# Kernel optimization log

Hardware: AMD Instinct MI355X
Metric: run time of the kernel (lower is better)

Reference implementation:

```python
import jax, jax.numpy as jnp
import numpy as np

H = 2048      # hidden_size
DM = 4096     # intermediate_size
N = 16        # ssm state size
K = 4         # conv kernel
R = 128       # time_step_rank
B_SZ = 1
L = 1024


def setup_inputs() -> dict:
    key = jax.random.key(0)
    ks = jax.random.split(key, 10)
    s = 0.02
    hidden_states = jax.random.normal(ks[0], (B_SZ, L, H), dtype=jnp.float32)
    W_in = jax.random.normal(ks[1], (2 * DM, H), dtype=jnp.float32) * s
    conv_w = jax.random.normal(ks[2], (DM, 1, K), dtype=jnp.float32) * 0.3
    conv_b = jax.random.normal(ks[3], (DM,), dtype=jnp.float32) * 0.1
    W_x = jax.random.normal(ks[4], (R + 2 * N, DM), dtype=jnp.float32) * s
    W_dt = jax.random.normal(ks[5], (DM, R), dtype=jnp.float32) * s
    b_dt = jax.random.normal(ks[6], (DM,), dtype=jnp.float32) * 0.1
    # A_log init: log(arange(1..N)) broadcast over channels (per __init__)
    A_log = jnp.broadcast_to(jnp.log(jnp.arange(1, N + 1, dtype=jnp.float32))[None, :], (DM, N)).copy()
    D_param = jnp.ones((DM,), dtype=jnp.float32)
    W_out = jax.random.normal(ks[7], (H, DM), dtype=jnp.float32) * s
    return {"hidden_states": hidden_states, "W_in": W_in, "conv_w": conv_w,
            "conv_b": conv_b, "W_x": W_x, "W_dt": W_dt, "b_dt": b_dt,
            "A_log": A_log, "D_param": D_param, "W_out": W_out}


def reference(hidden_states, W_in, conv_w, conv_b, W_x, W_dt, b_dt, A_log, D_param, W_out):
    # in_proj then chunk into hidden / gate (torch chunks dim=1 after transpose)
    proj = hidden_states @ W_in.T                     # [B, L, 2D]
    h, gate = proj[..., :DM], proj[..., DM:]          # each [B, L, D]
    # depthwise causal conv1d, padding K-1 then truncate to L (left-pad == same)
    h_cl = jnp.transpose(h, (0, 2, 1))                # [B, D, L]
    hc = jax.lax.conv_general_dilated(
        h_cl, conv_w, window_strides=(1,), padding=[(K - 1, 0)],
        dimension_numbers=("NCH", "OIH", "NCH"), feature_group_count=DM)
    hc = jax.nn.silu(hc + conv_b[None, :, None])      # [B, D, L]
    hc_ld = jnp.transpose(hc, (0, 2, 1))              # [B, L, D]
    # x_proj -> dt, B, C
    ssm_p = hc_ld @ W_x.T                             # [B, L, R+2N]
    ts, Bm, Cm = ssm_p[..., :R], ssm_p[..., R:R + N], ssm_p[..., R + N:]
    dt = jax.nn.softplus(ts @ W_dt.T + b_dt)          # [B, L, D]
    A = -jnp.exp(A_log)                               # [D, N]
    dA = jnp.exp(dt[:, :, :, None] * A[None, None, :, :])            # [B, L, D, N]
    dBu = dt[:, :, :, None] * Bm[:, :, None, :] * hc_ld[:, :, :, None]  # [B, L, D, N]
    # selective scan over time: state = dA*state + dBu; y = <state, C>
    def step(state, inp):
        dA_t, dBu_t, C_t = inp                        # [B,D,N],[B,D,N],[B,N]
        state = dA_t * state + dBu_t
        y = jnp.einsum("bdn,bn->bd", state, C_t)
        return state, y
    init = jnp.zeros((hidden_states.shape[0], DM, N), dtype=hidden_states.dtype)
    _, ys = jax.lax.scan(step, init,
                         (jnp.swapaxes(dA, 0, 1), jnp.swapaxes(dBu, 0, 1), jnp.swapaxes(Cm, 0, 1)))
    y = jnp.transpose(ys, (1, 0, 2))                  # [B, L, D]
    y = y + hc_ld * D_param[None, None, :]            # skip via D
    y = y * jax.nn.silu(gate)                         # gating
    return y @ W_out.T                                # [B, L, H]
```

## Files before the change

### kernel.cpp

```cpp
#include <hip/hip_runtime.h>
#include <math.h>

#define AS1 __attribute__((address_space(1)))
#define AS3 __attribute__((address_space(3)))

typedef __attribute__((ext_vector_type(8))) short short8;
typedef __attribute__((ext_vector_type(4))) float f32x4;

#define WAITV(n) asm volatile("s_waitcnt vmcnt(" #n ")" ::: "memory")
#define BARRIER() asm volatile("s_barrier" ::: "memory")

static __device__ __forceinline__ unsigned short f2bf(float f) {
    unsigned u = __float_as_uint(f);
    unsigned r = (u + 0x7fffu + ((u >> 16) & 1u)) >> 16;
    return (unsigned short)r;
}

__global__ __launch_bounds__(256) void cvt_f32_bf16(const float* __restrict__ src,
                                                    unsigned short* __restrict__ dst,
                                                    int n4) {
    int i = blockIdx.x * 256 + threadIdx.x;
    int stride = gridDim.x * 256;
    for (; i < n4; i += stride) {
        float4 v = ((const float4*)src)[i];
        ushort4 o;
        o.x = f2bf(v.x); o.y = f2bf(v.y); o.z = f2bf(v.z); o.w = f2bf(v.w);
        ((ushort4*)dst)[i] = o;
    }
}

__global__ __launch_bounds__(256) void cvt_ts(const float* __restrict__ ssmp,
                                              unsigned short* __restrict__ ts) {
    int i = blockIdx.x * 256 + threadIdx.x;
    int t = i >> 5, c4 = (i & 31) * 4;
    float4 v = *(const float4*)&ssmp[t * 160 + c4];
    ushort4 o;
    o.x = f2bf(v.x); o.y = f2bf(v.y); o.z = f2bf(v.z); o.w = f2bf(v.w);
    *(ushort4*)&ts[t * 128 + c4] = o;
}

__global__ __launch_bounds__(256) void conv_silu(const float* __restrict__ h,
                                                 const float* __restrict__ cw,
                                                 const float* __restrict__ cb,
                                                 float* __restrict__ hc_f,
                                                 unsigned short* __restrict__ hc_bf) {
    int idx = blockIdx.x * 256 + threadIdx.x;
    int d = idx & 4095, t = idx >> 12;
    float acc = cb[d];
    float4 w = *(const float4*)&cw[d * 4];
    const float* wp = (const float*)&w;
#pragma unroll
    for (int k = 0; k < 4; ++k) {
        int tt = t + k - 3;
        if (tt >= 0) acc += h[tt * 4096 + d] * wp[k];
    }
    float s = acc / (1.f + __expf(-acc));
    hc_f[idx] = s;
    hc_bf[idx] = f2bf(s);
}

enum { P_SPLIT = 0, P_ATOMIC = 1 };

template <int EPI>
__global__ __launch_bounds__(512, 2)
void gemm8p(const short* __restrict__ A, const short* __restrict__ B,
            float* __restrict__ C0, float* __restrict__ C1,
            int N, int K, int kchunk) {
    __shared__ short lds[2 * 24576];

    const int tid = threadIdx.x;
    const int wv = tid >> 6, ln = tid & 63;
    const int lr = ln & 15, kg = ln >> 4;
    const int wm = wv >> 2, wn = wv & 3;

    const int nwg = gridDim.x;
    const int bid = blockIdx.x;
    const int swz = (bid & 7) * (nwg >> 3) + (bid >> 3);
    const int by = swz & 7, bx = swz >> 3;
    const int m0 = by * 128;
    const int n0 = bx * 256;
    const int kbeg = blockIdx.z * kchunk;
    const int NT = kchunk >> 6;

    f32x4 acc[4][4];
#pragma unroll
    for (int mi = 0; mi < 4; ++mi)
#pragma unroll
        for (int ni = 0; ni < 4; ++ni) acc[mi][ni] = (f32x4){0.f, 0.f, 0.f, 0.f};

    const short* Abase = A + (size_t)m0 * K + kbeg;
    const short* Bbase = B + (size_t)n0 * K + kbeg;

#define STAGE(kt, b)                                                          \
    {                                                                         \
        short* lbase = &lds[(b) * 24576];                                     \
        _Pragma("unroll")                                                     \
        for (int r = 0; r < 2; ++r) {                                         \
            int c = r * 512 + tid;                                            \
            int row = c >> 3, cb8 = (c & 7) << 4;                             \
            int scb = cb8 ^ ((row & 7) << 4);                                 \
            const short* src = Abase + (size_t)row * K + (kt) * 64 + (scb >> 1); \
            short* dst = lbase + (r * 512 + wv * 64) * 8;                     \
            __builtin_amdgcn_global_load_lds((const AS1 void*)src,            \
                                             (AS3 void*)dst, 16, 0, 0);       \
        }                                                                     \
        _Pragma("unroll")                                                     \
        for (int r = 0; r < 4; ++r) {                                         \
            int c = r * 512 + tid;                                            \
            int row = c >> 3, cb8 = (c & 7) << 4;                             \
            int scb = cb8 ^ ((row & 7) << 4);                                 \
            const short* src = Bbase + (size_t)row * K + (kt) * 64 + (scb >> 1); \
            short* dst = lbase + 8192 + (r * 512 + wv * 64) * 8;              \
            __builtin_amdgcn_global_load_lds((const AS1 void*)src,            \
                                             (AS3 void*)dst, 16, 0, 0);       \
        }                                                                     \
    }

    STAGE(0, 0);

    for (int kt = 0; kt < NT; ++kt) {
        const int b = kt & 1;
        if (kt + 1 < NT) STAGE(kt + 1, b ^ 1);
        if (kt + 1 < NT) { WAITV(6); } else { WAITV(0); }
        BARRIER();
        {
            const short* la = &lds[b * 24576];
            const short* lb = la + 8192;
#pragma unroll
            for (int ks = 0; ks < 2; ++ks) {
                short8 av[4], bv[4];
#pragma unroll
                for (int mi = 0; mi < 4; ++mi) {
                    int row = wm * 64 + mi * 16 + lr;
                    int col = (ks * 32 + kg * 8) ^ ((row & 7) << 3);
                    av[mi] = *(const short8*)&la[row * 64 + col];
                }
#pragma unroll
                for (int ni = 0; ni < 4; ++ni) {
                    int row = wn * 64 + ni * 16 + lr;
                    int col = (ks * 32 + kg * 8) ^ ((row & 7) << 3);
                    bv[ni] = *(const short8*)&lb[row * 64 + col];
                }
                __builtin_amdgcn_s_setprio(1);
#pragma unroll
                for (int mi = 0; mi < 4; ++mi)
#pragma unroll
                    for (int ni = 0; ni < 4; ++ni)
                        acc[mi][ni] = __builtin_amdgcn_mfma_f32_16x16x32_bf16(
                            av[mi], bv[ni], acc[mi][ni], 0, 0, 0);
                __builtin_amdgcn_s_setprio(0);
            }
        }
        BARRIER();
    }
#undef STAGE

#pragma unroll
    for (int mi = 0; mi < 4; ++mi) {
        int crow0 = m0 + wm * 64 + mi * 16 + kg * 4;
#pragma unroll
        for (int ni = 0; ni < 4; ++ni) {
            int ccol = n0 + wn * 64 + ni * 16 + lr;
#pragma unroll
            for (int i = 0; i < 4; ++i) {
                float v = acc[mi][ni][i];
                size_t crow = (size_t)(crow0 + i);
                if constexpr (EPI == P_SPLIT) {
                    if (ccol < 4096) C0[crow * 4096 + ccol] = v;
                    else C1[crow * 4096 + (ccol - 4096)] = v;
                } else {
                    atomicAdd(&C0[crow * N + ccol], v);
                }
            }
        }
    }
}

enum { EPI_PLAIN = 0, EPI_SPLIT = 1, EPI_ATOMIC = 2, EPI_SOFTPLUS = 3 };

template <int BM, int EPI>
__global__ __launch_bounds__(256)
void gemm_bt(const short* __restrict__ A, const short* __restrict__ B,
             float* __restrict__ C, float* __restrict__ C2,
             const float* __restrict__ bias,
             int M, int N, int K, int ldc, int kcLen) {
    __shared__ short A_lds[BM * 32];
    __shared__ short B_lds[128 * 32];
    const int tid = threadIdx.x;
    const int wv = tid >> 6, ln = tid & 63;
    const int lr = ln & 15, kg = ln >> 4;
    const int m0 = blockIdx.y * BM;
    const int n0 = blockIdx.x * 128;
    const int kbeg = blockIdx.z * kcLen;
    const int kend = kbeg + kcLen;
    const int wm = wv >> 1, wn = wv & 1;
    constexpr int MR = BM / 32;

    f32x4 acc[MR][4];
#pragma unroll
    for (int mi = 0; mi < MR; ++mi)
#pragma unroll
        for (int ni = 0; ni < 4; ++ni) acc[mi][ni] = (f32x4){0.f, 0.f, 0.f, 0.f};

    const int arow = tid >> 2;
    const int kq8 = (tid & 3) * 8;

    for (int k0 = kbeg; k0 < kend; k0 += 32) {
#pragma unroll
        for (int r = 0; r < BM / 64; ++r) {
            const short* srcA = A + (size_t)(m0 + r * 64 + arow) * K + (k0 + kq8);
            short* dstA = &A_lds[(r * 64 + wv * 16) * 32];
            __builtin_amdgcn_global_load_lds((const AS1 void*)srcA, (AS3 void*)dstA, 16, 0, 0);
        }
#pragma unroll
        for (int r = 0; r < 2; ++r) {
            int brow = n0 + r * 64 + arow;
            if (brow > N - 1) brow = N - 1;
            const short* srcB = B + (size_t)brow * K + (k0 + kq8);
            short* dstB = &B_lds[(r * 64 + wv * 16) * 32];
            __builtin_amdgcn_global_load_lds((const AS1 void*)srcB, (AS3 void*)dstB, 16, 0, 0);
        }
        __syncthreads();

        short8 av[MR], bv[4];
#pragma unroll
        for (int mi = 0; mi < MR; ++mi)
            av[mi] = *(const short8*)&A_lds[(wm * (BM / 2) + mi * 16 + lr) * 32 + kg * 8];
#pragma unroll
        for (int ni = 0; ni < 4; ++ni)
            bv[ni] = *(const short8*)&B_lds[(wn * 64 + ni * 16 + lr) * 32 + kg * 8];
#pragma unroll
        for (int mi = 0; mi < MR; ++mi)
#pragma unroll
            for (int ni = 0; ni < 4; ++ni)
                acc[mi][ni] = __builtin_amdgcn_mfma_f32_16x16x32_bf16(av[mi], bv[ni], acc[mi][ni], 0, 0, 0);
        __syncthreads();
    }

#pragma unroll
    for (int mi = 0; mi < MR; ++mi) {
        int crow0 = m0 + wm * (BM / 2) + mi * 16 + kg * 4;
#pragma unroll
        for (int ni = 0; ni < 4; ++ni) {
            int ccol = n0 + wn * 64 + ni * 16 + lr;
#pragma unroll
            for (int i = 0; i < 4; ++i) {
                float v = acc[mi][ni][i];
                size_t crow = (size_t)(crow0 + i);
                if constexpr (EPI == EPI_PLAIN) {
                    C[crow * ldc + ccol] = v;
                } else if constexpr (EPI == EPI_SPLIT) {
                    if (ccol < 4096) C[crow * 4096 + ccol] = v;
                    else C2[crow * 4096 + (ccol - 4096)] = v;
                } else if constexpr (EPI == EPI_ATOMIC) {
                    if (ccol < N) atomicAdd(&C[crow * ldc + ccol], v);
                } else {
                    float x = v + bias[ccol];
                    C[crow * ldc + ccol] = fmaxf(x, 0.f) + log1pf(__expf(-fabsf(x)));
                }
            }
        }
    }
}

#define CLEN 16
#define NCH 64

__global__ __launch_bounds__(256)
void scan_p1(const float* __restrict__ dt, const float* __restrict__ hc,
             const float* __restrict__ ssmp, const float* __restrict__ A_log,
             float* __restrict__ Sbuf, float* __restrict__ dtsum) {
    const int tid = threadIdx.x;
    const int c = blockIdx.x & (NCH - 1);
    const int db = blockIdx.x >> 6;
    const int d = db * 256 + tid;
    const int t0 = c * CLEN;

    float Ac[16];
#pragma unroll
    for (int i = 0; i < 4; ++i) {
        float4 v = *(const float4*)&A_log[d * 16 + i * 4];
        Ac[i*4+0] = -__expf(v.x); Ac[i*4+1] = -__expf(v.y);
        Ac[i*4+2] = -__expf(v.z); Ac[i*4+3] = -__expf(v.w);
    }

    __shared__ float sB[CLEN][16];
    sB[tid >> 4][tid & 15] = ssmp[(t0 + (tid >> 4)) * 160 + 128 + (tid & 15)];
    __syncthreads();

    float st[16];
#pragma unroll
    for (int n = 0; n < 16; ++n) st[n] = 0.f;
    float ds = 0.f;

    for (int tt = 0; tt < CLEN; ++tt) {
        float dtv = dt[(size_t)(t0 + tt) * 4096 + d];
        float hcv = hc[(size_t)(t0 + tt) * 4096 + d];
        float du = dtv * hcv;
        ds += dtv;
#pragma unroll
        for (int n = 0; n < 16; ++n) {
            float dA = __expf(dtv * Ac[n]);
            st[n] = fmaf(dA, st[n], du * sB[tt][n]);
        }
    }

    float* o = Sbuf + ((size_t)c * 4096 + d) * 16;
#pragma unroll
    for (int i = 0; i < 4; ++i)
        *(float4*)&o[i * 4] = make_float4(st[i*4], st[i*4+1], st[i*4+2], st[i*4+3]);
    dtsum[c * 4096 + d] = ds;
}

__global__ __launch_bounds__(256)
void scan_p2(const float* __restrict__ A_log, const float* __restrict__ dtsum,
             float* __restrict__ S) {
    const int idx = blockIdx.x * 256 + threadIdx.x;
    const int d = idx >> 4;
    const float Ac = -__expf(A_log[idx]);
    float s = 0.f;
    for (int c = 0; c < NCH; ++c) {
        size_t o = (size_t)c * 65536 + idx;
        float sl = S[o];
        float P = __expf(Ac * dtsum[c * 4096 + d]);
        S[o] = s;
        s = fmaf(P, s, sl);
    }
}

__global__ __launch_bounds__(256)
void scan_p3(const float* __restrict__ dt, const float* __restrict__ hc,
             const float* __restrict__ ssmp, const float* __restrict__ A_log,
             const float* __restrict__ Dp, const float* __restrict__ gate,
             const float* __restrict__ Sinit, unsigned short* __restrict__ y_bf) {
    const int tid = threadIdx.x;
    const int c = blockIdx.x & (NCH - 1);
    const int db = blockIdx.x >> 6;
    const int d = db * 256 + tid;
    const int t0 = c * CLEN;

    float Ac[16];
#pragma unroll
    for (int i = 0; i < 4; ++i) {
        float4 v = *(const float4*)&A_log[d * 16 + i * 4];
        Ac[i*4+0] = -__expf(v.x); Ac[i*4+1] = -__expf(v.y);
        Ac[i*4+2] = -__expf(v.z); Ac[i*4+3] = -__expf(v.w);
    }
    const float Dcoef = Dp[d];

    __shared__ float sB[CLEN][16], sC[CLEN][16];
    {
        int tt = tid >> 4, nn = tid & 15;
        sB[tt][nn] = ssmp[(t0 + tt) * 160 + 128 + nn];
        sC[tt][nn] = ssmp[(t0 + tt) * 160 + 144 + nn];
    }
    __syncthreads();

    float st[16];
    {
        const float* si = Sinit + ((size_t)c * 4096 + d) * 16;
#pragma unroll
        for (int i = 0; i < 4; ++i) {
            float4 v = *(const float4*)&si[i * 4];
            st[i*4] = v.x; st[i*4+1] = v.y; st[i*4+2] = v.z; st[i*4+3] = v.w;
        }
    }

    for (int tt = 0; tt < CLEN; ++tt) {
        size_t g = (size_t)(t0 + tt) * 4096 + d;
        float dtv = dt[g];
        float hcv = hc[g];
        float du = dtv * hcv;
        float p[16];
#pragma unroll
        for (int n = 0; n < 16; ++n) {
            float dA = __expf(dtv * Ac[n]);
            st[n] = fmaf(dA, st[n], du * sB[tt][n]);
            p[n] = st[n] * sC[tt][n];
        }
#pragma unroll
        for (int n = 0; n < 8; ++n) p[n] += p[n + 8];
#pragma unroll
        for (int n = 0; n < 4; ++n) p[n] += p[n + 4];
        p[0] += p[2]; p[1] += p[3];
        float csum = p[0] + p[1];
        float gv = gate[g];
        float yv = (csum + hcv * Dcoef) * (gv / (1.f + __expf(-gv)));
        y_bf[g] = f2bf(yv);
    }
}

extern "C" void kernel_launch(void* const* d_in, const int* in_sizes, int n_in,
                              void* d_out, int out_size, void* d_ws, size_t ws_size,
                              hipStream_t stream) {
    (void)in_sizes; (void)n_in; (void)out_size; (void)ws_size;
    const float* hidden = (const float*)d_in[0];
    const float* W_in   = (const float*)d_in[1];
    const float* conv_w = (const float*)d_in[2];
    const float* conv_b = (const float*)d_in[3];
    const float* W_x    = (const float*)d_in[4];
    const float* W_dt   = (const float*)d_in[5];
    const float* b_dt   = (const float*)d_in[6];
    const float* A_log  = (const float*)d_in[7];
    const float* D_p    = (const float*)d_in[8];
    const float* W_out  = (const float*)d_in[9];
    float* out = (float*)d_out;

    char* w = (char*)d_ws;
    unsigned short* hid_bf = (unsigned short*)w;  w += (size_t)1024 * 2048 * 2;
    unsigned short* Wbig   = (unsigned short*)w;  w += (size_t)8192 * 2048 * 2;
    float* h_buf           = (float*)w;           w += (size_t)1024 * 4096 * 4;
    float* gate            = (float*)w;           w += (size_t)1024 * 4096 * 4;
    float* hc_f            = (float*)w;           w += (size_t)1024 * 4096 * 4;
    unsigned short* hc_bf  = (unsigned short*)w;  w += (size_t)1024 * 4096 * 2;
    float* ssmp            = (float*)w;           w += (size_t)1024 * 160 * 4;
    unsigned short* ts_bf  = (unsigned short*)w;  w += (size_t)1024 * 128 * 2;
    unsigned short* Wx_bf  = (unsigned short*)w;  w += (size_t)160 * 4096 * 2;
    unsigned short* Wdt_bf = (unsigned short*)w;  w += (size_t)4096 * 128 * 2;
    unsigned short* y_bf   = (unsigned short*)w;  w += (size_t)1024 * 4096 * 2;
    float* Sbuf            = (float*)w;           w += (size_t)NCH * 4096 * 16 * 4;
    float* dtsum           = (float*)w;           w += (size_t)NCH * 4096 * 4;

    hipMemsetAsync(ssmp, 0, (size_t)1024 * 160 * 4, stream);
    hipMemsetAsync(out, 0, (size_t)1024 * 2048 * 4, stream);

    cvt_f32_bf16<<<2048, 256, 0, stream>>>(hidden, hid_bf, 1024 * 2048 / 4);
    cvt_f32_bf16<<<4096, 256, 0, stream>>>(W_in, Wbig, 8192 * 2048 / 4);
    cvt_f32_bf16<<<640, 256, 0, stream>>>(W_x, Wx_bf, 160 * 4096 / 4);
    cvt_f32_bf16<<<512, 256, 0, stream>>>(W_dt, Wdt_bf, 4096 * 128 / 4);

    gemm8p<P_SPLIT><<<dim3(256, 1, 1), 512, 0, stream>>>(
        (const short*)hid_bf, (const short*)Wbig, h_buf, gate, 8192, 2048, 2048);

    conv_silu<<<16384, 256, 0, stream>>>(h_buf, conv_w, conv_b, hc_f, hc_bf);

    cvt_f32_bf16<<<2048, 256, 0, stream>>>(W_out, Wbig, 2048 * 4096 / 4);

    gemm_bt<128, EPI_ATOMIC><<<dim3(2, 8, 16), 256, 0, stream>>>(
        (const short*)hc_bf, (const short*)Wx_bf, ssmp, nullptr, nullptr,
        1024, 160, 4096, 160, 256);

    cvt_ts<<<128, 256, 0, stream>>>(ssmp, ts_bf);

    gemm_bt<128, EPI_SOFTPLUS><<<dim3(32, 8, 1), 256, 0, stream>>>(
        (const short*)ts_bf, (const short*)Wdt_bf, h_buf, nullptr, b_dt,
        1024, 4096, 128, 4096, 128);

    scan_p1<<<NCH * 16, 256, 0, stream>>>(h_buf, hc_f, ssmp, A_log, Sbuf, dtsum);
    scan_p2<<<256, 256, 0, stream>>>(A_log, dtsum, Sbuf);
    scan_p3<<<NCH * 16, 256, 0, stream>>>(h_buf, hc_f, ssmp, A_log, D_p, gate, Sbuf, y_bf);

    gemm8p<P_ATOMIC><<<dim3(64, 1, 4), 512, 0, stream>>>(
        (const short*)y_bf, (const short*)Wbig, out, nullptr, 2048, 4096, 1024);
}
```

Measured before the change: 236.3 us.

## Enlarge GEMM tiles to 256x256 with split-K atomics and batch scan_p2 loads

The bf16 MFMA GEMM tile grows from 128x256 to 256x256 (8x4 accumulators per wave, 64KB LDS per buffer) to raise data reuse per loaded byte. Both big GEMMs now use split-K (2 and 8 slices) with atomicAdd epilogues, which needs extra memsets of h_buf and gate. scan_p2 preloads all chunk states and decay factors before the serial recurrence. The cost is more register pressure, lower occupancy (128KB LDS at launch bound 2 may not fit), and atomic write traffic.

```diff
diff --git a/kernel.cpp b/kernel.cpp
--- a/kernel.cpp
+++ b/kernel.cpp
@@ -59,14 +59,14 @@
     hc_bf[idx] = f2bf(s);
 }
 
-enum { P_SPLIT = 0, P_ATOMIC = 1 };
+enum { G_SPLIT = 0, G_ATOMIC = 1 };
 
 template <int EPI>
 __global__ __launch_bounds__(512, 2)
-void gemm8p(const short* __restrict__ A, const short* __restrict__ B,
-            float* __restrict__ C0, float* __restrict__ C1,
-            int N, int K, int kchunk) {
-    __shared__ short lds[2 * 24576];
+void gemm256(const short* __restrict__ A, const short* __restrict__ B,
+             float* __restrict__ C0, float* __restrict__ C1,
+             int N, int K, int kchunk) {
+    __shared__ short lds[2 * 32768];
 
     const int tid = threadIdx.x;
     const int wv = tid >> 6, ln = tid & 63;
@@ -76,15 +76,14 @@
     const int nwg = gridDim.x;
     const int bid = blockIdx.x;
     const int swz = (bid & 7) * (nwg >> 3) + (bid >> 3);
-    const int by = swz & 7, bx = swz >> 3;
-    const int m0 = by * 128;
-    const int n0 = bx * 256;
+    const int by = swz & 3, bx = swz >> 2;
+    const int m0 = by * 256, n0 = bx * 256;
     const int kbeg = blockIdx.z * kchunk;
     const int NT = kchunk >> 6;
 
-    f32x4 acc[4][4];
-#pragma unroll
-    for (int mi = 0; mi < 4; ++mi)
+    f32x4 acc[8][4];
+#pragma unroll
+    for (int mi = 0; mi < 8; ++mi)
 #pragma unroll
         for (int ni = 0; ni < 4; ++ni) acc[mi][ni] = (f32x4){0.f, 0.f, 0.f, 0.f};
 
@@ -93,9 +92,9 @@
 
 #define STAGE(kt, b)                                                          \
     {                                                                         \
-        short* lbase = &lds[(b) * 24576];                                     \
+        short* lbase = &lds[(b) * 32768];                                     \
         _Pragma("unroll")                                                     \
-        for (int r = 0; r < 2; ++r) {                                         \
+        for (int r = 0; r < 4; ++r) {                                         \
             int c = r * 512 + tid;                                            \
             int row = c >> 3, cb8 = (c & 7) << 4;                             \
             int scb = cb8 ^ ((row & 7) << 4);                                 \
@@ -110,7 +109,7 @@
             int row = c >> 3, cb8 = (c & 7) << 4;                             \
             int scb = cb8 ^ ((row & 7) << 4);                                 \
             const short* src = Bbase + (size_t)row * K + (kt) * 64 + (scb >> 1); \
-            short* dst = lbase + 8192 + (r * 512 + wv * 64) * 8;              \
+            short* dst = lbase + 16384 + (r * 512 + wv * 64) * 8;             \
             __builtin_amdgcn_global_load_lds((const AS1 void*)src,            \
                                              (AS3 void*)dst, 16, 0, 0);       \
         }                                                                     \
@@ -121,34 +120,38 @@
     for (int kt = 0; kt < NT; ++kt) {
         const int b = kt & 1;
         if (kt + 1 < NT) STAGE(kt + 1, b ^ 1);
-        if (kt + 1 < NT) { WAITV(6); } else { WAITV(0); }
+        if (kt + 1 < NT) { WAITV(8); } else { WAITV(0); }
         BARRIER();
         {
-            const short* la = &lds[b * 24576];
-            const short* lb = la + 8192;
+            const short* la = &lds[b * 32768];
+            const short* lb = la + 16384;
 #pragma unroll
             for (int ks = 0; ks < 2; ++ks) {
-                short8 av[4], bv[4];
-#pragma unroll
-                for (int mi = 0; mi < 4; ++mi) {
-                    int row = wm * 64 + mi * 16 + lr;
-                    int col = (ks * 32 + kg * 8) ^ ((row & 7) << 3);
-                    av[mi] = *(const short8*)&la[row * 64 + col];
-                }
+                short8 bv[4];
 #pragma unroll
                 for (int ni = 0; ni < 4; ++ni) {
                     int row = wn * 64 + ni * 16 + lr;
                     int col = (ks * 32 + kg * 8) ^ ((row & 7) << 3);
                     bv[ni] = *(const short8*)&lb[row * 64 + col];
                 }
-                __builtin_amdgcn_s_setprio(1);
-#pragma unroll
-                for (int mi = 0; mi < 4; ++mi)
-#pragma unroll
-                    for (int ni = 0; ni < 4; ++ni)
-                        acc[mi][ni] = __builtin_amdgcn_mfma_f32_16x16x32_bf16(
-                            av[mi], bv[ni], acc[mi][ni], 0, 0, 0);
-                __builtin_amdgcn_s_setprio(0);
+#pragma unroll
+                for (int mh = 0; mh < 2; ++mh) {
+                    short8 av[4];
+#pragma unroll
+                    for (int q = 0; q < 4; ++q) {
+                        int row = wm * 128 + (mh * 4 + q) * 16 + lr;
+                        int col = (ks * 32 + kg * 8) ^ ((row & 7) << 3);
+                        av[q] = *(const short8*)&la[row * 64 + col];
+                    }
+                    __builtin_amdgcn_s_setprio(1);
+#pragma unroll
+                    for (int q = 0; q < 4; ++q)
+#pragma unroll
+                        for (int ni = 0; ni < 4; ++ni)
+                            acc[mh * 4 + q][ni] = __builtin_amdgcn_mfma_f32_16x16x32_bf16(
+                                av[q], bv[ni], acc[mh * 4 + q][ni], 0, 0, 0);
+                    __builtin_amdgcn_s_setprio(0);
+                }
             }
         }
         BARRIER();
@@ -156,8 +159,8 @@
 #undef STAGE
 
 #pragma unroll
-    for (int mi = 0; mi < 4; ++mi) {
-        int crow0 = m0 + wm * 64 + mi * 16 + kg * 4;
+    for (int mi = 0; mi < 8; ++mi) {
+        int crow0 = m0 + wm * 128 + mi * 16 + kg * 4;
 #pragma unroll
         for (int ni = 0; ni < 4; ++ni) {
             int ccol = n0 + wn * 64 + ni * 16 + lr;
@@ -165,9 +168,9 @@
             for (int i = 0; i < 4; ++i) {
                 float v = acc[mi][ni][i];
                 size_t crow = (size_t)(crow0 + i);
-                if constexpr (EPI == P_SPLIT) {
-                    if (ccol < 4096) C0[crow * 4096 + ccol] = v;
-                    else C1[crow * 4096 + (ccol - 4096)] = v;
+                if constexpr (EPI == G_SPLIT) {
+                    if (ccol < 4096) atomicAdd(&C0[crow * 4096 + ccol], v);
+                    else atomicAdd(&C1[crow * 4096 + (ccol - 4096)], v);
                 } else {
                     atomicAdd(&C0[crow * N + ccol], v);
                 }
@@ -318,13 +321,18 @@
     const int idx = blockIdx.x * 256 + threadIdx.x;
     const int d = idx >> 4;
     const float Ac = -__expf(A_log[idx]);
+
+    float sl[NCH], Pv[NCH];
+#pragma unroll
+    for (int c = 0; c < NCH; ++c) sl[c] = S[(size_t)c * 65536 + idx];
+#pragma unroll
+    for (int c = 0; c < NCH; ++c) Pv[c] = __expf(Ac * dtsum[c * 4096 + d]);
+
     float s = 0.f;
+#pragma unroll
     for (int c = 0; c < NCH; ++c) {
-        size_t o = (size_t)c * 65536 + idx;
-        float sl = S[o];
-        float P = __expf(Ac * dtsum[c * 4096 + d]);
-        S[o] = s;
-        s = fmaf(P, s, sl);
+        S[(size_t)c * 65536 + idx] = s;
+        s = fmaf(Pv[c], s, sl[c]);
     }
 }
 
@@ -423,14 +431,16 @@
 
     hipMemsetAsync(ssmp, 0, (size_t)1024 * 160 * 4, stream);
     hipMemsetAsync(out, 0, (size_t)1024 * 2048 * 4, stream);
+    hipMemsetAsync(h_buf, 0, (size_t)1024 * 4096 * 4, stream);
+    hipMemsetAsync(gate, 0, (size_t)1024 * 4096 * 4, stream);
 
     cvt_f32_bf16<<<2048, 256, 0, stream>>>(hidden, hid_bf, 1024 * 2048 / 4);
     cvt_f32_bf16<<<4096, 256, 0, stream>>>(W_in, Wbig, 8192 * 2048 / 4);
     cvt_f32_bf16<<<640, 256, 0, stream>>>(W_x, Wx_bf, 160 * 4096 / 4);
     cvt_f32_bf16<<<512, 256, 0, stream>>>(W_dt, Wdt_bf, 4096 * 128 / 4);
 
-    gemm8p<P_SPLIT><<<dim3(256, 1, 1), 512, 0, stream>>>(
-        (const short*)hid_bf, (const short*)Wbig, h_buf, gate, 8192, 2048, 2048);
+    gemm256<G_SPLIT><<<dim3(128, 1, 2), 512, 0, stream>>>(
+        (const short*)hid_bf, (const short*)Wbig, h_buf, gate, 8192, 2048, 1024);
 
     conv_silu<<<16384, 256, 0, stream>>>(h_buf, conv_w, conv_b, hc_f, hc_bf);
 
@@ -450,6 +460,6 @@
     scan_p2<<<256, 256, 0, stream>>>(A_log, dtsum, Sbuf);
     scan_p3<<<NCH * 16, 256, 0, stream>>>(h_buf, hc_f, ssmp, A_log, D_p, gate, Sbuf, y_bf);
 
-    gemm8p<P_ATOMIC><<<dim3(64, 1, 4), 512, 0, stream>>>(
-        (const short*)y_bf, (const short*)Wbig, out, nullptr, 2048, 4096, 1024);
-}
+    gemm256<G_ATOMIC><<<dim3(32, 1, 8), 512, 0, stream>>>(
+        (const short*)y_bf, (const short*)Wbig, out, nullptr, 2048, 4096, 512);
+}
```

After: 320.3 us. 1.36x slower.

## Triple-buffer GEMM K loop and replace split-K atomics with partial-sum reduction

Applied to the files above, without the earlier changes.

The bf16 GEMM kernel moves from double to triple LDS buffering, prefetching two K tiles ahead with matching vmcnt waits. The split-K output projection writes partials into reused scratch buffers instead of using atomicAdd, followed by a separate vectorized reduce kernel, which also removes the output memset. scan_p2 hoists all chunk loads and exp computations ahead of the serial recurrence. The larger LDS footprint likely cuts occupancy to one block per CU, and the reduce adds an extra memory pass.

```diff
diff --git a/kernel.cpp b/kernel.cpp
--- a/kernel.cpp
+++ b/kernel.cpp
@@ -59,14 +59,34 @@
     hc_bf[idx] = f2bf(s);
 }
 
-enum { P_SPLIT = 0, P_ATOMIC = 1 };
+__global__ __launch_bounds__(256) void reduce4(const float* __restrict__ pA,
+                                               const float* __restrict__ pB,
+                                               float* __restrict__ out, int n4) {
+    int i = blockIdx.x * 256 + threadIdx.x;
+    int stride = gridDim.x * 256;
+    const size_t MN4 = (size_t)1024 * 2048 / 4;
+    for (; i < n4; i += stride) {
+        float4 a = ((const float4*)pA)[i];
+        float4 b = ((const float4*)pA)[i + MN4];
+        float4 c = ((const float4*)pB)[i];
+        float4 d = ((const float4*)pB)[i + MN4];
+        float4 o;
+        o.x = (a.x + b.x) + (c.x + d.x);
+        o.y = (a.y + b.y) + (c.y + d.y);
+        o.z = (a.z + b.z) + (c.z + d.z);
+        o.w = (a.w + b.w) + (c.w + d.w);
+        ((float4*)out)[i] = o;
+    }
+}
+
+enum { P_SPLIT = 0, P_PART = 1 };
 
 template <int EPI>
 __global__ __launch_bounds__(512, 2)
 void gemm8p(const short* __restrict__ A, const short* __restrict__ B,
             float* __restrict__ C0, float* __restrict__ C1,
             int N, int K, int kchunk) {
-    __shared__ short lds[2 * 24576];
+    __shared__ short lds[3 * 24576];
 
     const int tid = threadIdx.x;
     const int wv = tid >> 6, ln = tid & 63;
@@ -117,11 +137,14 @@
     }
 
     STAGE(0, 0);
+    if (NT > 1) STAGE(1, 1);
 
     for (int kt = 0; kt < NT; ++kt) {
-        const int b = kt & 1;
-        if (kt + 1 < NT) STAGE(kt + 1, b ^ 1);
-        if (kt + 1 < NT) { WAITV(6); } else { WAITV(0); }
+        const int b = kt % 3;
+        if (kt + 2 < NT) STAGE(kt + 2, (kt + 2) % 3);
+        int ahead = NT - 1 - kt;
+        if (ahead > 2) ahead = 2;
+        if (ahead == 2) { WAITV(12); } else if (ahead == 1) { WAITV(6); } else { WAITV(0); }
         BARRIER();
         {
             const short* la = &lds[b * 24576];
@@ -169,7 +192,9 @@
                     if (ccol < 4096) C0[crow * 4096 + ccol] = v;
                     else C1[crow * 4096 + (ccol - 4096)] = v;
                 } else {
-                    atomicAdd(&C0[crow * N + ccol], v);
+                    float* Cz = (blockIdx.z < 2 ? C0 : C1) +
+                                (size_t)(blockIdx.z & 1) * 1024 * 2048;
+                    Cz[crow * N + ccol] = v;
                 }
             }
         }
@@ -318,13 +343,18 @@
     const int idx = blockIdx.x * 256 + threadIdx.x;
     const int d = idx >> 4;
     const float Ac = -__expf(A_log[idx]);
+
+    float sl[NCH], Pv[NCH];
+#pragma unroll
+    for (int c = 0; c < NCH; ++c) sl[c] = S[(size_t)c * 65536 + idx];
+#pragma unroll
+    for (int c = 0; c < NCH; ++c) Pv[c] = __expf(Ac * dtsum[c * 4096 + d]);
+
     float s = 0.f;
+#pragma unroll
     for (int c = 0; c < NCH; ++c) {
-        size_t o = (size_t)c * 65536 + idx;
-        float sl = S[o];
-        float P = __expf(Ac * dtsum[c * 4096 + d]);
-        S[o] = s;
-        s = fmaf(P, s, sl);
+        S[(size_t)c * 65536 + idx] = s;
+        s = fmaf(Pv[c], s, sl[c]);
     }
 }
 
@@ -422,7 +452,6 @@
     float* dtsum           = (float*)w;           w += (size_t)NCH * 4096 * 4;
 
     hipMemsetAsync(ssmp, 0, (size_t)1024 * 160 * 4, stream);
-    hipMemsetAsync(out, 0, (size_t)1024 * 2048 * 4, stream);
 
     cvt_f32_bf16<<<2048, 256, 0, stream>>>(hidden, hid_bf, 1024 * 2048 / 4);
     cvt_f32_bf16<<<4096, 256, 0, stream>>>(W_in, Wbig, 8192 * 2048 / 4);
@@ -450,6 +479,7 @@
     scan_p2<<<256, 256, 0, stream>>>(A_log, dtsum, Sbuf);
     scan_p3<<<NCH * 16, 256, 0, stream>>>(h_buf, hc_f, ssmp, A_log, D_p, gate, Sbuf, y_bf);
 
-    gemm8p<P_ATOMIC><<<dim3(64, 1, 4), 512, 0, stream>>>(
-        (const short*)y_bf, (const short*)Wbig, out, nullptr, 2048, 4096, 1024);
-}
+    gemm8p<P_PART><<<dim3(64, 1, 4), 512, 0, stream>>>(
+        (const short*)y_bf, (const short*)Wbig, Sbuf, hc_f, 2048, 4096, 1024);
+    reduce4<<<2048, 256, 0, stream>>>(Sbuf, hc_f, out, 1024 * 2048 / 4);
+}
```

Measured after the change: 220.4 us. 6.7% less time.
